# Performance work log

Hardware: AMD Instinct MI355X
Metric: run time of the kernel (lower is better)

Reference implementation:

```python
import math
import jax, jax.numpy as jnp
import numpy as np

N, D, E, H = 4096, 512, 64, 8
LN_EPS = 1e-5


def setup_inputs() -> dict:
    key = jax.random.key(0)
    ks = jax.random.split(key, 6)
    return {
        "x": jax.random.normal(ks[0], (N, D), jnp.float32),
        "wq": jax.random.normal(ks[1], (H, D, E), jnp.float32) * 0.05,
        "wk": jax.random.normal(ks[2], (H, D, E), jnp.float32) * 0.05,
        "wv": jax.random.normal(ks[3], (H, D, E), jnp.float32) * 0.05,
        "w_mh": jax.random.normal(ks[4], (H * E, D), jnp.float32) * 0.05,
        "ln1_g": jnp.ones((D,), jnp.float32),
        "ln1_b": jnp.zeros((D,), jnp.float32),
        "ffn_w": jax.random.normal(ks[5], (D, D), jnp.float32) * 0.05,  # torch Linear weight [out,in]
        "ffn_b": jnp.zeros((D,), jnp.float32),
        "ln2_g": jnp.ones((D,), jnp.float32),
        "ln2_b": jnp.zeros((D,), jnp.float32),
    }


def _layernorm(y, g, b):
    m = y.mean(-1, keepdims=True)
    v = ((y - m) ** 2).mean(-1, keepdims=True)
    return (y - m) * jax.lax.rsqrt(v + LN_EPS) * g + b


def reference(x, wq, wk, wv, w_mh, ln1_g, ln1_b, ffn_w, ffn_b, ln2_g, ln2_b):
    dk = math.sqrt(wk.shape[-1])  # sqrt(embedding_size), as in the torch code
    q = jnp.einsum('nd,hde->hne', x, wq)  # [H,N,E]
    k = jnp.einsum('nd,hde->hne', x, wk)
    v = jnp.einsum('nd,hde->hne', x, wv)
    scores = jax.nn.softmax(jnp.einsum('hne,hme->hnm', q, k) / dk, axis=-1)  # [H,N,N]
    z = jnp.einsum('hnm,hme->hne', scores, v)  # [H,N,E]
    concat_z = jnp.transpose(z, (1, 0, 2)).reshape(x.shape[0], -1)  # [N, H*E]
    transformed_z = concat_z @ w_mh  # [N, D]
    normed_z = _layernorm(transformed_z + x, ln1_g, ln1_b)
    out = normed_z @ ffn_w.T + ffn_b  # nn.Linear
    return _layernorm(out + normed_z, ln2_g, ln2_b)
```

## Files before the change

### kernel.cpp

```cpp
#include <hip/hip_runtime.h>

#define NN 4096
#define DD 512
#define EE 64
#define HH 8

typedef _Float16 f16;
typedef f16 f16x4 __attribute__((ext_vector_type(4)));
typedef f16 f16x8 __attribute__((ext_vector_type(8)));
typedef float f32x4 __attribute__((ext_vector_type(4)));

__device__ __forceinline__ float hexp2(float x) { return __builtin_amdgcn_exp2f(x); }

__global__ __launch_bounds__(256) void cvt_kernel(const float* __restrict__ s, f16* __restrict__ d, int n)
{
    int i = (blockIdx.x * 256 + threadIdx.x) * 4;
    if (i < n) {
        float4 t = *(const float4*)(s + i);
        f16x4 h = { (f16)t.x, (f16)t.y, (f16)t.z, (f16)t.w };
        *(f16x4*)(d + i) = h;
    }
}

__global__ __launch_bounds__(256) void transpose_cvt_kernel(
    const float* __restrict__ src, f16* __restrict__ dst, int R, int C)
{
    __shared__ float t[32][33];
    const int z = blockIdx.z;
    src += (size_t)z * R * C;
    dst += (size_t)z * R * C;
    const int bx = blockIdx.x * 32;
    const int by = blockIdx.y * 32;
    const int tx = threadIdx.x & 31;
    const int ty = threadIdx.x >> 5;
    #pragma unroll
    for (int i = 0; i < 4; ++i) {
        int r = ty + i * 8;
        t[r][tx] = src[(size_t)(by + r) * C + bx + tx];
    }
    __syncthreads();
    #pragma unroll
    for (int i = 0; i < 4; ++i) {
        int c = ty + i * 8;
        dst[(size_t)(bx + c) * R + by + tx] = (f16)t[tx][c];
    }
}

__global__ __launch_bounds__(256) void qkv_mfma_kernel(
    const f16* __restrict__ A, const f16* __restrict__ BT,
    f16* __restrict__ qh, f16* __restrict__ kh, f16* __restrict__ vTh)
{
    __shared__ f16 As[64][72];
    __shared__ f16 Bs[64][72];
    const int tid = threadIdx.x;
    const int n0 = blockIdx.x * 64;
    const int cb = blockIdx.y;
    const int sel = cb >> 3, h = cb & 7;
    const f16* Arow = A + (size_t)n0 * DD;
    const f16* Brow = BT + (size_t)cb * 64 * DD;

    const int lane = tid & 63, wave = tid >> 6;
    const int l16 = lane & 15, quad = lane >> 4;
    const int m0 = wave * 16;

    f32x4 acc[4];
    #pragma unroll
    for (int t = 0; t < 4; ++t) acc[t] = (f32x4){0.f, 0.f, 0.f, 0.f};

    for (int kt = 0; kt < DD; kt += 64) {
        __syncthreads();
        #pragma unroll
        for (int i = 0; i < 2; ++i) {
            int idx = tid + i * 256;
            int r = idx >> 3, c8 = (idx & 7) * 8;
            *(f16x8*)(&As[r][c8]) = *(const f16x8*)(Arow + (size_t)r * DD + kt + c8);
            *(f16x8*)(&Bs[r][c8]) = *(const f16x8*)(Brow + (size_t)r * DD + kt + c8);
        }
        __syncthreads();
        #pragma unroll
        for (int kk = 0; kk < 64; kk += 32) {
            f16x8 a = *(const f16x8*)(&As[m0 + l16][kk + quad * 8]);
            #pragma unroll
            for (int t = 0; t < 4; ++t) {
                f16x8 b = *(const f16x8*)(&Bs[t * 16 + l16][kk + quad * 8]);
                acc[t] = __builtin_amdgcn_mfma_f32_16x16x32_f16(a, b, acc[t], 0, 0, 0);
            }
        }
    }

    if (sel == 2) {
        #pragma unroll
        for (int t = 0; t < 4; ++t) {
            int e = t * 16 + l16;
            #pragma unroll
            for (int r = 0; r < 4; ++r)
                vTh[((size_t)h * EE + e) * NN + n0 + m0 + quad * 4 + r] = (f16)acc[t][r];
        }
    } else {
        f16* o = (sel == 0) ? qh : kh;
        const float s = (sel == 0) ? 0.125f * 1.44269504088896f : 1.0f;
        #pragma unroll
        for (int r = 0; r < 4; ++r) {
            int row = n0 + m0 + quad * 4 + r;
            #pragma unroll
            for (int t = 0; t < 4; ++t)
                o[(size_t)h * NN * EE + (size_t)row * EE + t * 16 + l16] = (f16)(acc[t][r] * s);
        }
    }
}

#define BQ 64
#define BK 64
#define LK (BK + 12)

__global__ __launch_bounds__(256) void attn_mfma_kernel(
    const f16* __restrict__ q, const f16* __restrict__ k,
    const f16* __restrict__ vT, float* __restrict__ Opart, float* __restrict__ lpart)
{
    __shared__ f16 Ks[BK][LK];
    __shared__ f16 VsT[EE][LK];

    const int tid = threadIdx.x;
    const int h = blockIdx.y;
    const int n0 = blockIdx.x * BQ;
    const int sp = blockIdx.z;
    const int nsp = gridDim.z;
    const int wave = tid >> 6;
    const int lane = tid & 63;
    const int l16 = lane & 15;
    const int quad = lane >> 4;
    const int m0 = wave * 16;

    const f16* qh = q + (size_t)h * NN * EE;
    const f16* kh = k + (size_t)h * NN * EE;
    const f16* vh = vT + (size_t)h * NN * EE;

    f16x8 qf0 = *(const f16x8*)(qh + (size_t)(n0 + m0 + l16) * EE + quad * 8);
    f16x8 qf1 = *(const f16x8*)(qh + (size_t)(n0 + m0 + l16) * EE + 32 + quad * 8);

    float lp = 0.f;
    f32x4 O[4];
    #pragma unroll
    for (int t = 0; t < 4; ++t) O[t] = (f32x4){0.f, 0.f, 0.f, 0.f};

    const int span = NN / nsp;
    const int k_begin = sp * span;
    const int k_end = k_begin + span;

    const int srow = tid >> 3, sc8 = (tid & 7) * 8;
    const int srow2 = (tid + 256) >> 3, sc82 = ((tid + 256) & 7) * 8;
    #define KPERM(kk_) (((kk_) & 0x23) | (((kk_) & 0x04) << 2) | (((kk_) & 0x18) >> 1))
    const int prow1 = KPERM(srow), prow2 = KPERM(srow2);

    f16x8 kr0 = *(const f16x8*)(kh + (size_t)(k_begin + srow) * EE + sc8);
    f16x8 kr1 = *(const f16x8*)(kh + (size_t)(k_begin + srow2) * EE + sc82);
    f16x8 vr0 = *(const f16x8*)(vh + (size_t)srow * NN + k_begin + sc8);
    f16x8 vr1 = *(const f16x8*)(vh + (size_t)srow2 * NN + k_begin + sc82);

    for (int kt = k_begin; kt < k_end; kt += BK) {
        __syncthreads();
        *(f16x8*)(&Ks[prow1][sc8]) = kr0;
        *(f16x8*)(&Ks[prow2][sc82]) = kr1;
        *(f16x8*)(&VsT[srow][sc8]) = vr0;
        *(f16x8*)(&VsT[srow2][sc82]) = vr1;
        __syncthreads();

        if (kt + BK < k_end) {
            kr0 = *(const f16x8*)(kh + (size_t)(kt + BK + srow) * EE + sc8);
            kr1 = *(const f16x8*)(kh + (size_t)(kt + BK + srow2) * EE + sc82);
            vr0 = *(const f16x8*)(vh + (size_t)srow * NN + kt + BK + sc8);
            vr1 = *(const f16x8*)(vh + (size_t)srow2 * NN + kt + BK + sc82);
        }

        f32x4 st[4];
        #pragma unroll
        for (int t = 0; t < 4; ++t) {
            f16x8 a0 = *(const f16x8*)(&Ks[t * 16 + l16][quad * 8]);
            f16x8 a1 = *(const f16x8*)(&Ks[t * 16 + l16][32 + quad * 8]);
            f32x4 s = {0.f, 0.f, 0.f, 0.f};
            s = __builtin_amdgcn_mfma_f32_16x16x32_f16(a0, qf0, s, 0, 0, 0);
            s = __builtin_amdgcn_mfma_f32_16x16x32_f16(a1, qf1, s, 0, 0, 0);
            st[t] = s;
        }

        f16x8 bf[2];
        #pragma unroll
        for (int t = 0; t < 4; ++t) {
            float p0 = hexp2(st[t][0]);
            float p1 = hexp2(st[t][1]);
            float p2 = hexp2(st[t][2]);
            float p3 = hexp2(st[t][3]);
            lp += (p0 + p1) + (p2 + p3);
            f16x8& b = bf[t >> 1];
            const int o = (t & 1) * 4;
            b[o + 0] = (f16)p0; b[o + 1] = (f16)p1;
            b[o + 2] = (f16)p2; b[o + 3] = (f16)p3;
        }

        #pragma unroll
        for (int te = 0; te < 4; ++te) {
            f16x8 v0 = *(const f16x8*)(&VsT[te * 16 + l16][quad * 8]);
            f16x8 v1 = *(const f16x8*)(&VsT[te * 16 + l16][32 + quad * 8]);
            O[te] = __builtin_amdgcn_mfma_f32_16x16x32_f16(v0, bf[0], O[te], 0, 0, 0);
            O[te] = __builtin_amdgcn_mfma_f32_16x16x32_f16(v1, bf[1], O[te], 0, 0, 0);
        }
    }

    const int row = n0 + m0 + l16;
    lp += __shfl_xor(lp, 16);
    lp += __shfl_xor(lp, 32);
    if (quad == 0)
        lpart[(size_t)sp * HH * NN + (size_t)h * NN + row] = lp;
    #pragma unroll
    for (int te = 0; te < 4; ++te)
        *(f32x4*)(Opart + ((size_t)sp * NN + row) * DD + h * EE + te * 16 + quad * 4) = O[te];
}

__global__ __launch_bounds__(256) void attn_combine_kernel(
    const float* __restrict__ Opart, const float* __restrict__ lpart, f16* __restrict__ zh, int nsp)
{
    const size_t idx = ((size_t)blockIdx.x * 256 + threadIdx.x) * 8;
    const int n = (int)(idx >> 9);
    const int h = (int)((idx & 511) >> 6);
    float l = 0.f;
    for (int s = 0; s < nsp; ++s) l += lpart[(size_t)s * HH * NN + (size_t)h * NN + n];
    const float inv = 1.f / l;
    f32x4 a0 = {0.f,0.f,0.f,0.f}, a1 = {0.f,0.f,0.f,0.f};
    for (int s = 0; s < nsp; ++s) {
        a0 += *(const f32x4*)(Opart + (size_t)s * NN * DD + idx);
        a1 += *(const f32x4*)(Opart + (size_t)s * NN * DD + idx + 4);
    }
    f16x8 o;
    #pragma unroll
    for (int i = 0; i < 4; ++i) {
        o[i]     = (f16)(a0[i] * inv);
        o[i + 4] = (f16)(a1[i] * inv);
    }
    *(f16x8*)(zh + idx) = o;
}

__global__ __launch_bounds__(256) void gemm_mfma_kernel(
    const f16* __restrict__ A, const f16* __restrict__ BT,
    const float* __restrict__ bias, const float* __restrict__ resid32,
    const f16* __restrict__ resid16, float* __restrict__ out)
{
    __shared__ f16 As[64][72];
    __shared__ f16 Bs[64][72];
    const int tid = threadIdx.x;
    const int n0 = blockIdx.x * 64;
    const int j0 = blockIdx.y * 64;
    const f16* Arow = A + (size_t)n0 * DD;
    const f16* Brow = BT + (size_t)j0 * DD;

    const int lane = tid & 63, wave = tid >> 6;
    const int l16 = lane & 15, quad = lane >> 4;
    const int m0 = wave * 16;

    f32x4 acc[4];
    #pragma unroll
    for (int t = 0; t < 4; ++t) acc[t] = (f32x4){0.f, 0.f, 0.f, 0.f};

    for (int kt = 0; kt < DD; kt += 64) {
        __syncthreads();
        #pragma unroll
        for (int i = 0; i < 2; ++i) {
            int idx = tid + i * 256;
            int r = idx >> 3, c8 = (idx & 7) * 8;
            *(f16x8*)(&As[r][c8]) = *(const f16x8*)(Arow + (size_t)r * DD + kt + c8);
            *(f16x8*)(&Bs[r][c8]) = *(const f16x8*)(Brow + (size_t)r * DD + kt + c8);
        }
        __syncthreads();
        #pragma unroll
        for (int kk = 0; kk < 64; kk += 32) {
            f16x8 a = *(const f16x8*)(&As[m0 + l16][kk + quad * 8]);
            #pragma unroll
            for (int t = 0; t < 4; ++t) {
                f16x8 b = *(const f16x8*)(&Bs[t * 16 + l16][kk + quad * 8]);
                acc[t] = __builtin_amdgcn_mfma_f32_16x16x32_f16(a, b, acc[t], 0, 0, 0);
            }
        }
    }

    #pragma unroll
    for (int r = 0; r < 4; ++r) {
        int row = n0 + m0 + quad * 4 + r;
        #pragma unroll
        for (int t = 0; t < 4; ++t) {
            int col = j0 + t * 16 + l16;
            float v = acc[t][r];
            if (bias)    v += bias[col];
            if (resid32) v += resid32[(size_t)row * DD + col];
            if (resid16) v += (float)resid16[(size_t)row * DD + col];
            out[(size_t)row * DD + col] = v;
        }
    }
}

__global__ __launch_bounds__(256) void ln_kernel(
    const float* __restrict__ y, const float* __restrict__ g, const float* __restrict__ b,
    f16* __restrict__ oh, float* __restrict__ of)
{
    const int lane = threadIdx.x & 63, wave = threadIdx.x >> 6;
    const int row = blockIdx.x * 4 + wave;
    const float* yr = y + (size_t)row * DD;
    f32x4 v0 = *(const f32x4*)(yr + lane * 4);
    f32x4 v1 = *(const f32x4*)(yr + 256 + lane * 4);
    float s = (v0[0] + v0[1]) + (v0[2] + v0[3]) + (v1[0] + v1[1]) + (v1[2] + v1[3]);
    float q = (v0[0]*v0[0] + v0[1]*v0[1]) + (v0[2]*v0[2] + v0[3]*v0[3])
            + (v1[0]*v1[0] + v1[1]*v1[1]) + (v1[2]*v1[2] + v1[3]*v1[3]);
    #pragma unroll
    for (int o = 1; o < 64; o <<= 1) { s += __shfl_xor(s, o); q += __shfl_xor(q, o); }
    float mean = s * (1.f / DD);
    float var = q * (1.f / DD) - mean * mean;
    float inv = rsqrtf(var + 1e-5f);

    f32x4 g0 = *(const f32x4*)(g + lane * 4);
    f32x4 g1 = *(const f32x4*)(g + 256 + lane * 4);
    f32x4 b0 = *(const f32x4*)(b + lane * 4);
    f32x4 b1 = *(const f32x4*)(b + 256 + lane * 4);
    f32x4 o0, o1;
    #pragma unroll
    for (int i = 0; i < 4; ++i) {
        o0[i] = (v0[i] - mean) * inv * g0[i] + b0[i];
        o1[i] = (v1[i] - mean) * inv * g1[i] + b1[i];
    }
    if (oh) {
        f16x4 h0 = { (f16)o0[0], (f16)o0[1], (f16)o0[2], (f16)o0[3] };
        f16x4 h1 = { (f16)o1[0], (f16)o1[1], (f16)o1[2], (f16)o1[3] };
        *(f16x4*)(oh + (size_t)row * DD + lane * 4) = h0;
        *(f16x4*)(oh + (size_t)row * DD + 256 + lane * 4) = h1;
    }
    if (of) {
        *(f32x4*)(of + (size_t)row * DD + lane * 4) = o0;
        *(f32x4*)(of + (size_t)row * DD + 256 + lane * 4) = o1;
    }
}

extern "C" void kernel_launch(void* const* d_in, const int* in_sizes, int n_in,
                              void* d_out, int out_size, void* d_ws, size_t ws_size,
                              hipStream_t stream) {
    const float* x     = (const float*)d_in[0];
    const float* wq    = (const float*)d_in[1];
    const float* wk    = (const float*)d_in[2];
    const float* wv    = (const float*)d_in[3];
    const float* w_mh  = (const float*)d_in[4];
    const float* ln1_g = (const float*)d_in[5];
    const float* ln1_b = (const float*)d_in[6];
    const float* ffn_w = (const float*)d_in[7];
    const float* ffn_b = (const float*)d_in[8];
    const float* ln2_g = (const float*)d_in[9];
    const float* ln2_b = (const float*)d_in[10];
    float* out = (float*)d_out;

    const size_t poolHalfs = (size_t)3 * HH * EE * DD + 2 * (size_t)DD * DD
                           + 3 * (size_t)HH * NN * EE + 2 * (size_t)NN * DD;
    int SP = 2;
    {
        size_t need4 = ((size_t)4 * NN * DD + 4 * HH * NN) * 4 + poolHalfs * 2 + 1024;
        size_t need3 = ((size_t)3 * NN * DD + 3 * HH * NN) * 4 + poolHalfs * 2 + 1024;
        if (ws_size >= need4) SP = 4; else if (ws_size >= need3) SP = 3;
    }

    char* base = (char*)d_ws;
    float* Opart = (float*)base;
    float* lpart = Opart + (size_t)SP * NN * DD;
    f16* xh   = (f16*)base;
    float* y  = (float*)base;
    size_t regionA = ((size_t)SP * NN * DD + (size_t)SP * HH * NN) * sizeof(float);
    regionA = (regionA + 255) & ~(size_t)255;
    f16* p = (f16*)(base + regionA);
    f16* wqkvT  = p; p += (size_t)3 * HH * EE * DD;
    f16* wmhT   = p; p += (size_t)DD * DD;
    f16* ffnT   = p; p += (size_t)DD * DD;
    f16* qh     = p; p += (size_t)HH * NN * EE;
    f16* kh     = p; p += (size_t)HH * NN * EE;
    f16* vTh    = p; p += (size_t)HH * NN * EE;
    f16* zh     = p; p += (size_t)NN * DD;
    f16* nzh    = p; p += (size_t)NN * DD;

    cvt_kernel<<<dim3(NN * DD / 1024), 256, 0, stream>>>(x, xh, NN * DD);
    cvt_kernel<<<dim3(DD * DD / 1024), 256, 0, stream>>>(ffn_w, ffnT, DD * DD);
    transpose_cvt_kernel<<<dim3(EE / 32, DD / 32, HH), 256, 0, stream>>>(wq, wqkvT, DD, EE);
    transpose_cvt_kernel<<<dim3(EE / 32, DD / 32, HH), 256, 0, stream>>>(wk, wqkvT + (size_t)HH * EE * DD, DD, EE);
    transpose_cvt_kernel<<<dim3(EE / 32, DD / 32, HH), 256, 0, stream>>>(wv, wqkvT + (size_t)2 * HH * EE * DD, DD, EE);
    transpose_cvt_kernel<<<dim3(DD / 32, DD / 32, 1), 256, 0, stream>>>(w_mh, wmhT, DD, DD);

    qkv_mfma_kernel<<<dim3(NN / 64, 24), 256, 0, stream>>>(xh, wqkvT, qh, kh, vTh);
    attn_mfma_kernel<<<dim3(NN / BQ, HH, SP), 256, 0, stream>>>(qh, kh, vTh, Opart, lpart);
    attn_combine_kernel<<<dim3(NN * DD / 2048), 256, 0, stream>>>(Opart, lpart, zh, SP);
    gemm_mfma_kernel<<<dim3(NN / 64, DD / 64), 256, 0, stream>>>(zh, wmhT, nullptr, x, nullptr, y);
    ln_kernel<<<dim3(NN / 4), 256, 0, stream>>>(y, ln1_g, ln1_b, nzh, nullptr);
    gemm_mfma_kernel<<<dim3(NN / 64, DD / 64), 256, 0, stream>>>(nzh, ffnT, ffn_b, nullptr, nzh, y);
    ln_kernel<<<dim3(NN / 4), 256, 0, stream>>>(y, ln2_g, ln2_b, nullptr, out);
}
```

Baseline: 201.8 us.

## Use 32x32 MFMA tiles in attention with intra-block key split; fuse prep kernels

The attention kernel now uses 32x32x16 MFMA instructions. Each wave computes a 32-query by 32-key tile, and two waves split the 64 keys of each tile. Their partial outputs are combined through shared memory at the end, and the combine kernel sums twice as many partial row sums. The six separate convert/transpose preprocessing launches are merged into one multi-job kernel to cut launch overhead. In exchange there is an extra shared-memory reduction, larger lpart storage, and a changed LDS row permutation for bank-conflict avoidance.

After: 290.4 us. +43.9%, slower.

```diff
diff --git a/kernel.cpp b/kernel.cpp
--- a/kernel.cpp
+++ b/kernel.cpp
@@ -9,30 +9,15 @@
 typedef f16 f16x4 __attribute__((ext_vector_type(4)));
 typedef f16 f16x8 __attribute__((ext_vector_type(8)));
 typedef float f32x4 __attribute__((ext_vector_type(4)));
+typedef float f32x16 __attribute__((ext_vector_type(16)));
 
 __device__ __forceinline__ float hexp2(float x) { return __builtin_amdgcn_exp2f(x); }
 
-__global__ __launch_bounds__(256) void cvt_kernel(const float* __restrict__ s, f16* __restrict__ d, int n)
-{
-    int i = (blockIdx.x * 256 + threadIdx.x) * 4;
-    if (i < n) {
-        float4 t = *(const float4*)(s + i);
-        f16x4 h = { (f16)t.x, (f16)t.y, (f16)t.z, (f16)t.w };
-        *(f16x4*)(d + i) = h;
-    }
-}
-
-__global__ __launch_bounds__(256) void transpose_cvt_kernel(
-    const float* __restrict__ src, f16* __restrict__ dst, int R, int C)
+__device__ void tile_transpose_cvt(const float* __restrict__ src, f16* __restrict__ dst,
+                                   int R, int C, int bx, int by, int tid)
 {
     __shared__ float t[32][33];
-    const int z = blockIdx.z;
-    src += (size_t)z * R * C;
-    dst += (size_t)z * R * C;
-    const int bx = blockIdx.x * 32;
-    const int by = blockIdx.y * 32;
-    const int tx = threadIdx.x & 31;
-    const int ty = threadIdx.x >> 5;
+    const int tx = tid & 31, ty = tid >> 5;
     #pragma unroll
     for (int i = 0; i < 4; ++i) {
         int r = ty + i * 8;
@@ -43,6 +28,40 @@
     for (int i = 0; i < 4; ++i) {
         int c = ty + i * 8;
         dst[(size_t)(bx + c) * R + by + tx] = (f16)t[tx][c];
+    }
+}
+
+__global__ __launch_bounds__(256) void prep_kernel(
+    const float* __restrict__ x, const float* __restrict__ ffn_w,
+    const float* __restrict__ wq, const float* __restrict__ wk, const float* __restrict__ wv,
+    const float* __restrict__ w_mh,
+    f16* __restrict__ xh, f16* __restrict__ ffnT, f16* __restrict__ wqkvT, f16* __restrict__ wmhT)
+{
+    const int job = blockIdx.y;
+    const int tid = threadIdx.x;
+    if (job == 0) {
+        size_t i = ((size_t)blockIdx.x * 256 + tid) * 4;
+        const size_t step = (size_t)256 * 256 * 4;
+        for (; i < (size_t)NN * DD; i += step) {
+            float4 t = *(const float4*)(x + i);
+            f16x4 h = { (f16)t.x, (f16)t.y, (f16)t.z, (f16)t.w };
+            *(f16x4*)(xh + i) = h;
+        }
+    } else if (job == 1) {
+        size_t i = ((size_t)blockIdx.x * 256 + tid) * 4;
+        float4 t = *(const float4*)(ffn_w + i);
+        f16x4 h = { (f16)t.x, (f16)t.y, (f16)t.z, (f16)t.w };
+        *(f16x4*)(ffnT + i) = h;
+    } else if (job <= 4) {
+        const float* src = (job == 2) ? wq : (job == 3) ? wk : wv;
+        f16* dst = wqkvT + (size_t)(job - 2) * HH * EE * DD;
+        const int z = blockIdx.x >> 5;
+        const int tile = blockIdx.x & 31;
+        tile_transpose_cvt(src + (size_t)z * DD * EE, dst + (size_t)z * DD * EE,
+                           DD, EE, (tile & 1) * 32, (tile >> 1) * 32, tid);
+    } else {
+        const int tile = blockIdx.x;
+        tile_transpose_cvt(w_mh, wmhT, DD, DD, (tile & 15) * 32, (tile >> 4) * 32, tid);
     }
 }
 
@@ -117,8 +136,10 @@
     const f16* __restrict__ q, const f16* __restrict__ k,
     const f16* __restrict__ vT, float* __restrict__ Opart, float* __restrict__ lpart)
 {
-    __shared__ f16 Ks[BK][LK];
-    __shared__ f16 VsT[EE][LK];
+    __shared__ __align__(16) char smem[(size_t)(BK + EE) * LK * sizeof(f16)];
+    f16 (*Ks)[LK]  = (f16(*)[LK])smem;
+    f16 (*VsT)[LK] = (f16(*)[LK])(smem + (size_t)BK * LK * sizeof(f16));
+    float* red = (float*)smem;
 
     const int tid = threadIdx.x;
     const int h = blockIdx.y;
@@ -127,21 +148,24 @@
     const int nsp = gridDim.z;
     const int wave = tid >> 6;
     const int lane = tid & 63;
-    const int l16 = lane & 15;
-    const int quad = lane >> 4;
-    const int m0 = wave * 16;
+    const int l32 = lane & 31;
+    const int u = lane >> 5;
+    const int qt2 = wave & 1;
+    const int kt2 = wave >> 1;
 
     const f16* qh = q + (size_t)h * NN * EE;
     const f16* kh = k + (size_t)h * NN * EE;
     const f16* vh = vT + (size_t)h * NN * EE;
 
-    f16x8 qf0 = *(const f16x8*)(qh + (size_t)(n0 + m0 + l16) * EE + quad * 8);
-    f16x8 qf1 = *(const f16x8*)(qh + (size_t)(n0 + m0 + l16) * EE + 32 + quad * 8);
+    f16x8 qf[4];
+    #pragma unroll
+    for (int ks = 0; ks < 4; ++ks)
+        qf[ks] = *(const f16x8*)(qh + (size_t)(n0 + qt2 * 32 + l32) * EE + ks * 16 + u * 8);
 
     float lp = 0.f;
-    f32x4 O[4];
-    #pragma unroll
-    for (int t = 0; t < 4; ++t) O[t] = (f32x4){0.f, 0.f, 0.f, 0.f};
+    f32x16 O[2];
+    #pragma unroll
+    for (int i = 0; i < 16; ++i) { O[0][i] = 0.f; O[1][i] = 0.f; }
 
     const int span = NN / nsp;
     const int k_begin = sp * span;
@@ -149,8 +173,8 @@
 
     const int srow = tid >> 3, sc8 = (tid & 7) * 8;
     const int srow2 = (tid + 256) >> 3, sc82 = ((tid + 256) & 7) * 8;
-    #define KPERM(kk_) (((kk_) & 0x23) | (((kk_) & 0x04) << 2) | (((kk_) & 0x18) >> 1))
-    const int prow1 = KPERM(srow), prow2 = KPERM(srow2);
+    #define KPERM2(kk_) (((kk_) & 0x33) | (((kk_) & 0x04) << 1) | (((kk_) & 0x08) >> 1))
+    const int prow1 = KPERM2(srow), prow2 = KPERM2(srow2);
 
     f16x8 kr0 = *(const f16x8*)(kh + (size_t)(k_begin + srow) * EE + sc8);
     f16x8 kr1 = *(const f16x8*)(kh + (size_t)(k_begin + srow2) * EE + sc82);
@@ -172,48 +196,68 @@
             vr1 = *(const f16x8*)(vh + (size_t)srow2 * NN + kt + BK + sc82);
         }
 
-        f32x4 st[4];
-        #pragma unroll
-        for (int t = 0; t < 4; ++t) {
-            f16x8 a0 = *(const f16x8*)(&Ks[t * 16 + l16][quad * 8]);
-            f16x8 a1 = *(const f16x8*)(&Ks[t * 16 + l16][32 + quad * 8]);
-            f32x4 s = {0.f, 0.f, 0.f, 0.f};
-            s = __builtin_amdgcn_mfma_f32_16x16x32_f16(a0, qf0, s, 0, 0, 0);
-            s = __builtin_amdgcn_mfma_f32_16x16x32_f16(a1, qf1, s, 0, 0, 0);
-            st[t] = s;
-        }
-
-        f16x8 bf[2];
-        #pragma unroll
-        for (int t = 0; t < 4; ++t) {
-            float p0 = hexp2(st[t][0]);
-            float p1 = hexp2(st[t][1]);
-            float p2 = hexp2(st[t][2]);
-            float p3 = hexp2(st[t][3]);
-            lp += (p0 + p1) + (p2 + p3);
-            f16x8& b = bf[t >> 1];
-            const int o = (t & 1) * 4;
-            b[o + 0] = (f16)p0; b[o + 1] = (f16)p1;
-            b[o + 2] = (f16)p2; b[o + 3] = (f16)p3;
-        }
-
-        #pragma unroll
-        for (int te = 0; te < 4; ++te) {
-            f16x8 v0 = *(const f16x8*)(&VsT[te * 16 + l16][quad * 8]);
-            f16x8 v1 = *(const f16x8*)(&VsT[te * 16 + l16][32 + quad * 8]);
-            O[te] = __builtin_amdgcn_mfma_f32_16x16x32_f16(v0, bf[0], O[te], 0, 0, 0);
-            O[te] = __builtin_amdgcn_mfma_f32_16x16x32_f16(v1, bf[1], O[te], 0, 0, 0);
-        }
-    }
-
-    const int row = n0 + m0 + l16;
-    lp += __shfl_xor(lp, 16);
+        f32x16 st;
+        #pragma unroll
+        for (int i = 0; i < 16; ++i) st[i] = 0.f;
+        #pragma unroll
+        for (int ks = 0; ks < 4; ++ks) {
+            f16x8 a = *(const f16x8*)(&Ks[kt2 * 32 + l32][ks * 16 + u * 8]);
+            st = __builtin_amdgcn_mfma_f32_32x32x16_f16(a, qf[ks], st, 0, 0, 0);
+        }
+
+        f16x8 bf0, bf1;
+        #pragma unroll
+        for (int r = 0; r < 8; ++r) {
+            float p = hexp2(st[r]);
+            lp += p;
+            bf0[r] = (f16)p;
+        }
+        #pragma unroll
+        for (int r = 0; r < 8; ++r) {
+            float p = hexp2(st[8 + r]);
+            lp += p;
+            bf1[r] = (f16)p;
+        }
+
+        #pragma unroll
+        for (int et = 0; et < 2; ++et) {
+            f16x8 a0 = *(const f16x8*)(&VsT[et * 32 + l32][kt2 * 32 + u * 8]);
+            f16x8 a1 = *(const f16x8*)(&VsT[et * 32 + l32][kt2 * 32 + 16 + u * 8]);
+            O[et] = __builtin_amdgcn_mfma_f32_32x32x16_f16(a0, bf0, O[et], 0, 0, 0);
+            O[et] = __builtin_amdgcn_mfma_f32_32x32x16_f16(a1, bf1, O[et], 0, 0, 0);
+        }
+    }
+
+    __syncthreads();
+    if (kt2 == 1) {
+        #pragma unroll
+        for (int et = 0; et < 2; ++et)
+            #pragma unroll
+            for (int r = 0; r < 16; ++r)
+                red[((qt2 * 2 + et) * 16 + r) * 64 + lane] = O[et][r];
+    }
+    __syncthreads();
+
     lp += __shfl_xor(lp, 32);
-    if (quad == 0)
-        lpart[(size_t)sp * HH * NN + (size_t)h * NN + row] = lp;
-    #pragma unroll
-    for (int te = 0; te < 4; ++te)
-        *(f32x4*)(Opart + ((size_t)sp * NN + row) * DD + h * EE + te * 16 + quad * 4) = O[te];
+    if (lane < 32)
+        lpart[((size_t)sp * 2 + kt2) * HH * NN + (size_t)h * NN + n0 + qt2 * 32 + lane] = lp;
+
+    if (kt2 == 0) {
+        #pragma unroll
+        for (int et = 0; et < 2; ++et)
+            #pragma unroll
+            for (int r = 0; r < 16; ++r)
+                O[et][r] += red[((qt2 * 2 + et) * 16 + r) * 64 + lane];
+        const int row = n0 + qt2 * 32 + l32;
+        float* obase = Opart + ((size_t)sp * NN + row) * DD + h * EE;
+        #pragma unroll
+        for (int et = 0; et < 2; ++et)
+            #pragma unroll
+            for (int g = 0; g < 4; ++g) {
+                f32x4 v = { O[et][g * 4 + 0], O[et][g * 4 + 1], O[et][g * 4 + 2], O[et][g * 4 + 3] };
+                *(f32x4*)(obase + et * 32 + 8 * g + 4 * u) = v;
+            }
+    }
 }
 
 __global__ __launch_bounds__(256) void attn_combine_kernel(
@@ -223,7 +267,7 @@
     const int n = (int)(idx >> 9);
     const int h = (int)((idx & 511) >> 6);
     float l = 0.f;
-    for (int s = 0; s < nsp; ++s) l += lpart[(size_t)s * HH * NN + (size_t)h * NN + n];
+    for (int s = 0; s < 2 * nsp; ++s) l += lpart[(size_t)s * HH * NN + (size_t)h * NN + n];
     const float inv = 1.f / l;
     f32x4 a0 = {0.f,0.f,0.f,0.f}, a1 = {0.f,0.f,0.f,0.f};
     for (int s = 0; s < nsp; ++s) {
@@ -356,8 +400,8 @@
                            + 3 * (size_t)HH * NN * EE + 2 * (size_t)NN * DD;
     int SP = 2;
     {
-        size_t need4 = ((size_t)4 * NN * DD + 4 * HH * NN) * 4 + poolHalfs * 2 + 1024;
-        size_t need3 = ((size_t)3 * NN * DD + 3 * HH * NN) * 4 + poolHalfs * 2 + 1024;
+        size_t need4 = ((size_t)4 * NN * DD + 8 * HH * NN) * 4 + poolHalfs * 2 + 1024;
+        size_t need3 = ((size_t)3 * NN * DD + 6 * HH * NN) * 4 + poolHalfs * 2 + 1024;
         if (ws_size >= need4) SP = 4; else if (ws_size >= need3) SP = 3;
     }
 
@@ -366,7 +410,7 @@
     float* lpart = Opart + (size_t)SP * NN * DD;
     f16* xh   = (f16*)base;
     float* y  = (float*)base;
-    size_t regionA = ((size_t)SP * NN * DD + (size_t)SP * HH * NN) * sizeof(float);
+    size_t regionA = ((size_t)SP * NN * DD + (size_t)2 * SP * HH * NN) * sizeof(float);
     regionA = (regionA + 255) & ~(size_t)255;
     f16* p = (f16*)(base + regionA);
     f16* wqkvT  = p; p += (size_t)3 * HH * EE * DD;
@@ -378,12 +422,8 @@
     f16* zh     = p; p += (size_t)NN * DD;
     f16* nzh    = p; p += (size_t)NN * DD;
 
-    cvt_kernel<<<dim3(NN * DD / 1024), 256, 0, stream>>>(x, xh, NN * DD);
-    cvt_kernel<<<dim3(DD * DD / 1024), 256, 0, stream>>>(ffn_w, ffnT, DD * DD);
-    transpose_cvt_kernel<<<dim3(EE / 32, DD / 32, HH), 256, 0, stream>>>(wq, wqkvT, DD, EE);
-    transpose_cvt_kernel<<<dim3(EE / 32, DD / 32, HH), 256, 0, stream>>>(wk, wqkvT + (size_t)HH * EE * DD, DD, EE);
-    transpose_cvt_kernel<<<dim3(EE / 32, DD / 32, HH), 256, 0, stream>>>(wv, wqkvT + (size_t)2 * HH * EE * DD, DD, EE);
-    transpose_cvt_kernel<<<dim3(DD / 32, DD / 32, 1), 256, 0, stream>>>(w_mh, wmhT, DD, DD);
+    prep_kernel<<<dim3(256, 6), 256, 0, stream>>>(x, ffn_w, wq, wk, wv, w_mh,
+                                                  xh, ffnT, wqkvT, wmhT);
 
     qkv_mfma_kernel<<<dim3(NN / 64, 24), 256, 0, stream>>>(xh, wqkvT, qh, kh, vTh);
     attn_mfma_kernel<<<dim3(NN / BQ, HH, SP), 256, 0, stream>>>(qh, kh, vTh, Opart, lpart);
```
